# Kernel tuning notes

Measured on AMD Instinct MI355X. Metric: run time of the kernel, lower is better.

The kernel has to match this reference:

```python
import jax, jax.numpy as jnp
import numpy as np

DECAY = 0.99
COMMIT = 0.25
EPS = 1e-5


def setup_inputs() -> dict:
    key = jax.random.key(0)
    k1, k2, k3 = jax.random.split(key, 3)
    B, H, W, D, K = 32, 32, 32, 64, 1024
    return {
        "z": jax.random.normal(k1, (B, H, W, D), dtype=jnp.float32),
        "embeddings": jax.random.normal(k2, (K, D), dtype=jnp.float32),
        "cluster_size": jnp.ones((K,), dtype=jnp.float32),
        "ema_embed": jax.random.normal(k3, (K, D), dtype=jnp.float32),
    }


def reference(z, embeddings, cluster_size, ema_embed):
    B, H, W, D = z.shape
    K = embeddings.shape[0]
    z_flat = z.reshape(-1, D)                      # [N, D]

    # squared L2 distances via expansion: ||z||^2 + ||e||^2 - 2 z e^T  -> [N, K]
    distances = (
        jnp.sum(z_flat * z_flat, axis=1, keepdims=True)
        + jnp.sum(embeddings * embeddings, axis=1)
        - 2.0 * z_flat @ embeddings.T
    )
    idx = jnp.argmin(distances, axis=1)            # [N]
    quantized = embeddings[idx].reshape(z.shape)   # gather, [B,H,W,D]

    # training-mode EMA update (one_hot^T matmuls expressed as segment sums)
    n_i = jax.ops.segment_sum(jnp.ones(z_flat.shape[0], z.dtype), idx, num_segments=K)
    dw = jax.ops.segment_sum(z_flat, idx, num_segments=K)          # [K, D]
    new_cluster = cluster_size * DECAY + n_i * (1.0 - DECAY)
    new_ema = ema_embed * DECAY + dw * (1.0 - DECAY)
    n = jnp.sum(new_cluster)
    new_cluster = (new_cluster + EPS) / (n + K * EPS) * n           # Laplace smoothing
    new_embeddings = new_ema / new_cluster[:, None]

    loss = COMMIT * jnp.mean((z - jax.lax.stop_gradient(quantized)) ** 2)
    q_ste = z + jax.lax.stop_gradient(quantized - z)                # straight-through

    quantized_vectors = jnp.transpose(q_ste, (0, 3, 1, 2))          # [B, D, H, W]
    quantized_indices = idx.reshape(B, H, W)[:, None, :, :]         # [B, 1, H, W]
    return quantized_vectors, quantized_indices, loss, new_embeddings, new_cluster, new_ema
```

## Files before the change

### kernel.cpp

```cpp
#include <hip/hip_runtime.h>


typedef unsigned short u16;
typedef u16 us8 __attribute__((ext_vector_type(8)));
typedef float f4 __attribute__((ext_vector_type(4)));

#define WS_FZ    0
#define WS_FE    1
#define WS_FCS   2
#define WS_FEMA  3
#define WS_LOSS  4
#define WS_CSSUM 5

__device__ __forceinline__ float b2f(u16 u) {
    union { unsigned int i; float f; } x; x.i = ((unsigned int)u) << 16; return x.f;
}
__device__ __forceinline__ int swzE32(int d, int c) {
    return d * 32 + (c ^ ((((d) >> 2) & 7) << 2));
}
__device__ __forceinline__ int swzZ(int d, int c) {
    int cb = (c >> 2) ^ (c >> 5);
    int cc = ((cb & 31) << 2) | (c & 3);
    return d * 128 + (cc ^ ((((d) >> 2) & 7) << 2));
}

__global__ __launch_bounds__(256) void k_init(
    const u16* z, const u16* e, const u16* cs, const u16* ema,
    float* __restrict__ ws, float* __restrict__ esqp,
    float* __restrict__ dwp, long long zeroN, int K)
{
    __shared__ int flg[4];
    __shared__ float csred[256];
    const int tid = threadIdx.x;
    const int w = tid >> 6, l = tid & 63;
    const u16* p = (w == 0) ? z : (w == 1) ? e : (w == 2) ? cs : ema;
    int cnt = 0;
    #pragma unroll
    for (int t = 0; t < 4; ++t) {
        unsigned hb = (p[(l * 4 + t) * 2] >> 8) & 0x7F;
        cnt += (hb >= 0x3A && hb <= 0x41) ? 1 : 0;
    }
    #pragma unroll
    for (int off = 32; off; off >>= 1) cnt += __shfl_down(cnt, off);
    if (l == 0) flg[w] = (cnt < 128) ? 1 : 0;
    __syncthreads();
    if (blockIdx.x == 0) {
        if (tid < 4) ((int*)ws)[tid] = flg[tid];
        if (tid == 4) ws[WS_LOSS] = 0.0f;
    }
    const int fe = flg[1];
    const int fcs = flg[2];

    {
        const int gwave = (blockIdx.x * 256 + tid) >> 6;
        const int nwave = (gridDim.x * 256) >> 6;
        for (int code = gwave; code < K; code += nwave) {
            float v = fe ? ((const float*)e)[(size_t)code * 64 + l]
                         : b2f(e[(size_t)code * 64 + l]);
            float pq = v * v;
            asm volatile("" : "+v"(pq));
            float r[8];
            #pragma unroll
            for (int j = 0; j < 8; ++j) r[j] = __shfl(pq, j);
            #pragma unroll
            for (int t = 1; t < 8; ++t)
                #pragma unroll
                for (int j = 0; j < 8; ++j) r[j] += __shfl(pq, 8 * t + j);
            float s = ((r[0] + r[1]) + (r[2] + r[3])) + ((r[4] + r[5]) + (r[6] + r[7]));
            if (l == 0) esqp[code] = s;
        }
    }
    {
        long long g = (long long)blockIdx.x * 256 + tid;
        long long stride = (long long)gridDim.x * 256;
        for (long long i = g; i < zeroN; i += stride) dwp[i] = 0.0f;
    }
    if (blockIdx.x == 0) {
        float partial = 0.f;
        for (int k0 = tid; k0 < K; k0 += 256)
            partial += fcs ? ((const float*)cs)[k0] : b2f(cs[k0]);
        csred[tid] = partial;
        __syncthreads();
        for (int s = 128; s; s >>= 1) {
            if (tid < s) csred[tid] += csred[tid + s];
            __syncthreads();
        }
        if (tid == 0) ws[WS_CSSUM] = csred[0];
    }
}

__global__ __launch_bounds__(512, 4) void k_main(
    const u16* __restrict__ z, const u16* __restrict__ e,
    const float* __restrict__ esqp,
    float* __restrict__ ws, float* __restrict__ out,
    float* __restrict__ dwp,
    int K, int offIdx, long long outSize)
{
    __shared__ __align__(16) float z_t[64 * 128];
    __shared__ __align__(16) float e_t[4 * 32 * 64];
    __shared__ float esq_l[2048];
    __shared__ float z2_l[64];
    __shared__ int   idx_l[64];

    const int tid = threadIdx.x;
    const int cg  = tid >> 7;
    const int lt  = tid & 127;
    const int mtg = lt & 15;
    const int ktg = lt >> 4;
    const int pbase = blockIdx.x * 64;
    const int* wsi = (const int*)ws;
    const int fz = wsi[WS_FZ];
    const int fe = wsi[WS_FE];
    const int h = K >> 7;

    for (int i = tid; i < K; i += 512) esq_l[i] = esqp[i];

    if (fz) {
        const f4* z4 = (const f4*)((const float*)z + (size_t)pbase * 64);
        for (int i = tid; i < 1024; i += 512) {
            f4 v = z4[i];
            int m = i >> 4, d4 = (i & 15) * 4;
            z_t[swzZ(d4 + 0, m)] = v[0];
            z_t[swzZ(d4 + 1, m)] = v[1];
            z_t[swzZ(d4 + 2, m)] = v[2];
            z_t[swzZ(d4 + 3, m)] = v[3];
        }
    } else {
        const us8* z8 = (const us8*)(z + (size_t)pbase * 64);
        for (int i = tid; i < 512; i += 512) {
            us8 v = z8[i];
            int m = i >> 3, d8 = (i & 7) * 8;
            #pragma unroll
            for (int t = 0; t < 8; ++t) z_t[swzZ(d8 + t, m)] = b2f(v[t]);
        }
    }
    __syncthreads();
    if (tid < 64) {
        float r[8];
        #pragma unroll
        for (int j = 0; j < 8; ++j) {
            float v = z_t[swzZ(j, tid)]; float p = v * v;
            asm volatile("" : "+v"(p)); r[j] = p;
        }
        #pragma unroll
        for (int t = 1; t < 8; ++t)
            #pragma unroll
            for (int j = 0; j < 8; ++j) {
                float v = z_t[swzZ(8 * t + j, tid)]; float p = v * v;
                asm volatile("" : "+v"(p)); r[j] += p;
            }
        z2_l[tid] = ((r[0] + r[1]) + (r[2] + r[3])) + ((r[4] + r[5]) + (r[6] + r[7]));
    }

    float bestd[4] = {INFINITY, INFINITY, INFINITY, INFINITY};
    int   besti[4] = {0, 0, 0, 0};
    float* et = e_t + cg * 2048;

    f4  fb[4];
    us8 hb[2];
    {
        int kc0 = cg * h;
        if (fe) {
            const f4* e4 = (const f4*)((const float*)e + (size_t)kc0 * 2048);
            #pragma unroll
            for (int t = 0; t < 4; ++t) fb[t] = e4[lt + 128 * t];
        } else {
            const us8* e8 = (const us8*)(e + (size_t)kc0 * 2048);
            #pragma unroll
            for (int t = 0; t < 2; ++t) hb[t] = e8[lt + 128 * t];
        }
    }

    for (int c = 0; c < h; ++c) {
        const int kc = cg * h + c;
        if (fe) {
            #pragma unroll
            for (int t = 0; t < 4; ++t) {
                int i = lt + 128 * t;
                int kl = i >> 4, d4 = (i & 15) * 4;
                et[swzE32(d4 + 0, kl)] = fb[t][0];
                et[swzE32(d4 + 1, kl)] = fb[t][1];
                et[swzE32(d4 + 2, kl)] = fb[t][2];
                et[swzE32(d4 + 3, kl)] = fb[t][3];
            }
        } else {
            #pragma unroll
            for (int t = 0; t < 2; ++t) {
                int i = lt + 128 * t;
                int kl = i >> 3, d8 = (i & 7) * 8;
                #pragma unroll
                for (int s = 0; s < 8; ++s) et[swzE32(d8 + s, kl)] = b2f(hb[t][s]);
            }
        }
        if (c + 1 < h) {
            if (fe) {
                const f4* e4 = (const f4*)((const float*)e + (size_t)(kc + 1) * 2048);
                #pragma unroll
                for (int t = 0; t < 4; ++t) fb[t] = e4[lt + 128 * t];
            } else {
                const us8* e8 = (const us8*)(e + (size_t)(kc + 1) * 2048);
                #pragma unroll
                for (int t = 0; t < 2; ++t) hb[t] = e8[lt + 128 * t];
            }
        }
        __syncthreads();

        float acc[4][4] = {};
        for (int d0 = 0; d0 < 64; d0 += 4) {
            f4 za[4], ea[4];
            #pragma unroll
            for (int j = 0; j < 4; ++j) {
                int d = d0 + j;
                za[j] = *(const f4*)&z_t[swzZ(d, mtg * 4)];
                ea[j] = *(const f4*)&et[swzE32(d, ktg * 4)];
            }
            #pragma unroll
            for (int j = 0; j < 4; ++j) {
                #pragma unroll
                for (int a = 0; a < 4; ++a)
                    #pragma unroll
                    for (int b = 0; b < 4; ++b)
                        acc[a][b] += za[j][a] * ea[j][b];
            }
        }
        __syncthreads();

        #pragma unroll
        for (int a = 0; a < 4; ++a) {
            float z2 = z2_l[mtg * 4 + a];
            #pragma unroll
            for (int b = 0; b < 4; ++b) {
                float e2 = esq_l[kc * 32 + ktg * 4 + b];
                float dist = (z2 + e2) - 2.0f * acc[a][b];
                int kg = kc * 32 + ktg * 4 + b;
                if (dist < bestd[a]) { bestd[a] = dist; besti[a] = kg; }
            }
        }
    }

    __syncthreads();

    #pragma unroll
    for (int mask = 16; mask <= 32; mask <<= 1) {
        #pragma unroll
        for (int a = 0; a < 4; ++a) {
            float od = __shfl_xor(bestd[a], mask);
            int   oi = __shfl_xor(besti[a], mask);
            if (od < bestd[a] || (od == bestd[a] && oi < besti[a])) {
                bestd[a] = od; besti[a] = oi;
            }
        }
    }
    float* red_d = esq_l;
    int*   red_i = (int*)(esq_l + 576);
    if ((lt & 63) < 16) {
        int slot = cg * 2 + (lt >> 6);
        #pragma unroll
        for (int a = 0; a < 4; ++a) {
            red_d[(mtg * 4 + a) * 9 + slot] = bestd[a];
            red_i[(mtg * 4 + a) * 9 + slot] = besti[a];
        }
    }
    __syncthreads();

    if (tid < 64) {
        float bd = red_d[tid * 9]; int bi = red_i[tid * 9];
        #pragma unroll
        for (int t = 1; t < 8; ++t) {
            float dv = red_d[tid * 9 + t]; int iv = red_i[tid * 9 + t];
            if (dv < bd || (dv == bd && iv < bi)) { bd = dv; bi = iv; }
        }
        idx_l[tid] = bi;
        long long oi = (long long)offIdx + pbase + tid;
        if (oi < outSize) out[oi] = (float)bi;
    }
    __syncthreads();

    const int m = tid & 63;
    const int w = tid >> 6;
    const int p = pbase + m;
    const int b = p >> 10;
    const int hw = p & 1023;
    const int kidx = idx_l[m];
    float* zt2 = e_t;
    float lsum = 0.f;
    #pragma unroll
    for (int dd = 0; dd < 8; ++dd) {
        int d = w + 8 * dd;
        float zv = z_t[swzZ(d, m)];
        float q  = fe ? ((const float*)e)[(size_t)kidx * 64 + d]
                      : b2f(e[(size_t)kidx * 64 + d]);
        float df = zv - q;
        lsum += df * df;
        float qs = zv + (q - zv);
        long long qi = (long long)b * 65536 + d * 1024 + hw;
        if (qi < outSize) out[qi] = qs;
        zt2[m * 65 + d] = zv;
    }
    #pragma unroll
    for (int off = 32; off; off >>= 1) lsum += __shfl_down(lsum, off);
    if ((tid & 63) == 0) atomicAdd(&ws[WS_LOSS], lsum);
    __syncthreads();

    {
        const int wv = tid >> 6, lane = tid & 63;
        #pragma unroll
        for (int it = 0; it < 8; ++it) {
            int mm = wv * 8 + it;
            int kk = idx_l[mm];
            float zv = zt2[mm * 65 + lane];
            atomicAdd(&dwp[(size_t)kk * 64 + lane], zv);
            if (lane == 0) atomicAdd(&dwp[(size_t)K * 64 + kk], 1.0f);
        }
    }
}

__global__ __launch_bounds__(256) void k_fin(
    const u16* __restrict__ cs, const u16* __restrict__ ema,
    const float* __restrict__ ws, const float* __restrict__ dwp,
    float* __restrict__ out, int K, int N,
    long long offLoss, long long outSize, float lossScale)
{
    const int* wsi = (const int*)ws;
    const int fcs = wsi[WS_FCS], fema = wsi[WS_FEMA];
    const int i = blockIdx.x * 256 + threadIdx.x;
    const long long offEmb = offLoss + 1;
    const long long offCl  = offEmb + (long long)K * 64;
    const long long offEma = offCl + K;
    const float nsum = 0.99f * ws[WS_CSSUM] + 0.01f * (float)N;
    const float keps = (float)K * 1e-5f;

    float cnt = 0.f, dw = 0.f, csv = 0.f, ev = 0.f;
    int k = 0, d = 0;
    const int ok = (i < K * 64);
    if (ok) {
        k = i >> 6; d = i & 63;
        dw  = dwp[i];
        cnt = dwp[(size_t)K * 64 + k];
        csv = fcs ? ((const float*)cs)[k] : b2f(cs[k]);
        ev  = fema ? ((const float*)ema)[i] : b2f(ema[i]);
    }
    __syncthreads();
    if (ok) {
        float c  = csv * 0.99f + cnt * 0.01f;
        float sm = (c + 1e-5f) / (nsum + keps) * nsum;
        float ne = ev * 0.99f + dw * 0.01f;
        if (offEma + i < outSize) out[offEma + i] = ne;
        if (offEmb + i < outSize) out[offEmb + i] = ne / sm;
        if (d == 0 && offCl + k < outSize) out[offCl + k] = sm;
    }
    if (blockIdx.x == 0 && threadIdx.x == 0 && offLoss < outSize)
        out[offLoss] = 0.25f * (ws[WS_LOSS] * lossScale);
}

extern "C" void kernel_launch(void* const* d_in, const int* in_sizes, int n_in,
                              void* d_out, int out_size, void* d_ws, size_t ws_size,
                              hipStream_t stream) {
    long long sz[4] = {0, 0, 0, 0};
    for (int i = 0; i < n_in && i < 4; ++i) sz[i] = in_sizes[i];
    int icl = 0, iz = 0;
    for (int i = 1; i < 4; ++i) { if (sz[i] < sz[icl]) icl = i; if (sz[i] > sz[iz]) iz = i; }
    int ip[2], np = 0;
    for (int i = 0; i < 4; ++i) if (i != icl && i != iz && np < 2) ip[np++] = i;
    long long K = sz[icl], KD = (np == 2) ? sz[ip[0]] : 0;
    int derivOK = (n_in == 4 && np == 2 && icl != iz && sz[ip[0]] == sz[ip[1]] &&
                   K > 0 && KD % K == 0);
    long long D = derivOK ? KD / K : 64;
    long long N = (derivOK && D > 0 && sz[iz] % D == 0) ? sz[iz] / D : 32768;
    int ie, iema;
    if (!derivOK) { iz = 0; ie = 1; icl = 2; iema = 3; N = 32768; K = 1024; D = 64; }
    else if (icl > ip[0] && icl < ip[1]) { ie = ip[0]; iema = ip[1]; }
    else { iema = ip[0]; ie = ip[1]; }

    int fastOK = (D == 64) && (N % 1024 == 0) && (K % 256 == 0) &&
                 (K >= 512) && (K <= 2048);
    if (!fastOK) { N = 32768; K = 1024; }

    long long offIdx = N * 64, offLoss = offIdx + N;
    long long offEmb = offLoss + 1, offCl = offEmb + K * 64, offEma = offCl + K;

    float* out = (float*)d_out;
    float* ws = (float*)d_ws;

    long long rep = K * 65;
    float *esqp, *dwp;
    if ((long long)ws_size >= (8 + K + rep) * 4) {
        esqp = ws + 8; dwp = ws + 8 + K;
    } else {
        esqp = out + offEma; dwp = out + offEmb;
    }

    const u16* z   = (const u16*)d_in[iz];
    const u16* e   = (const u16*)d_in[ie];
    const u16* cs  = (const u16*)d_in[icl];
    const u16* ema = (const u16*)d_in[iema];

    float lossScale = (float)(1.0 / (double)(N * 64));

    k_init<<<64, 256, 0, stream>>>(z, e, cs, ema, ws, esqp, dwp, rep, (int)K);
    k_main<<<(int)(N / 64), 512, 0, stream>>>(z, e, esqp, ws, out, dwp,
                                              (int)K, (int)offIdx, (long long)out_size);
    k_fin<<<(int)((K * 64 + 255) / 256), 256, 0, stream>>>(cs, ema, ws, dwp, out,
                                                           (int)K, (int)N, offLoss,
                                                           (long long)out_size, lossScale);
}
```

Baseline: 170.9 us.

## Give each wavefront its own codebook slice to drop per-chunk block barriers

The codebook split moves from four 128-thread groups handling 32-entry chunks to eight 64-lane wavefronts, each owning a private 16-entry staging tile. Since each tile is written and read only by its own wavefront, the two __syncthreads per chunk iteration are removed, and single barriers are added after the z-norm computation and before the cross-wave reduction. Chunk count per wave doubles and each chunk has half the codebook columns, so per-chunk loads and argmin updates are amortised over less math. Correctness relies on lockstep execution within a wavefront in place of explicit barriers around the LDS tile.

```diff
diff --git a/kernel.cpp b/kernel.cpp
--- a/kernel.cpp
+++ b/kernel.cpp
@@ -15,8 +15,8 @@
 __device__ __forceinline__ float b2f(u16 u) {
     union { unsigned int i; float f; } x; x.i = ((unsigned int)u) << 16; return x.f;
 }
-__device__ __forceinline__ int swzE32(int d, int c) {
-    return d * 32 + (c ^ ((((d) >> 2) & 7) << 2));
+__device__ __forceinline__ int swz16(int d, int c) {
+    return d * 16 + (c ^ ((((d) >> 2) & 3) << 2));
 }
 __device__ __forceinline__ int swzZ(int d, int c) {
     int cb = (c >> 2) ^ (c >> 5);
@@ -97,16 +97,16 @@
     int K, int offIdx, long long outSize)
 {
     __shared__ __align__(16) float z_t[64 * 128];
-    __shared__ __align__(16) float e_t[4 * 32 * 64];
+    __shared__ __align__(16) float e_t[8 * 16 * 64];
     __shared__ float esq_l[2048];
     __shared__ float z2_l[64];
     __shared__ int   idx_l[64];
 
     const int tid = threadIdx.x;
-    const int cg  = tid >> 7;
-    const int lt  = tid & 127;
-    const int mtg = lt & 15;
-    const int ktg = lt >> 4;
+    const int wv  = tid >> 6;
+    const int lane = tid & 63;
+    const int mtg = lane & 15;
+    const int ktg = lane >> 4;
     const int pbase = blockIdx.x * 64;
     const int* wsi = (const int*)ws;
     const int fz = wsi[WS_FZ];
@@ -151,59 +151,57 @@
             }
         z2_l[tid] = ((r[0] + r[1]) + (r[2] + r[3])) + ((r[4] + r[5]) + (r[6] + r[7]));
     }
+    __syncthreads();
 
     float bestd[4] = {INFINITY, INFINITY, INFINITY, INFINITY};
     int   besti[4] = {0, 0, 0, 0};
-    float* et = e_t + cg * 2048;
+    float* et = e_t + wv * 1024;
+    const int kc0 = wv * h;
 
     f4  fb[4];
     us8 hb[2];
-    {
-        int kc0 = cg * h;
+    if (fe) {
+        const f4* e4 = (const f4*)((const float*)e + (size_t)kc0 * 1024);
+        #pragma unroll
+        for (int t = 0; t < 4; ++t) fb[t] = e4[lane + 64 * t];
+    } else {
+        const us8* e8 = (const us8*)(e + (size_t)kc0 * 1024);
+        #pragma unroll
+        for (int t = 0; t < 2; ++t) hb[t] = e8[lane + 64 * t];
+    }
+
+    for (int c = 0; c < h; ++c) {
+        const int kc = kc0 + c;
         if (fe) {
-            const f4* e4 = (const f4*)((const float*)e + (size_t)kc0 * 2048);
-            #pragma unroll
-            for (int t = 0; t < 4; ++t) fb[t] = e4[lt + 128 * t];
+            #pragma unroll
+            for (int t = 0; t < 4; ++t) {
+                int i = lane + 64 * t;
+                int kl = i >> 4, d4 = (i & 15) * 4;
+                et[swz16(d4 + 0, kl)] = fb[t][0];
+                et[swz16(d4 + 1, kl)] = fb[t][1];
+                et[swz16(d4 + 2, kl)] = fb[t][2];
+                et[swz16(d4 + 3, kl)] = fb[t][3];
+            }
         } else {
-            const us8* e8 = (const us8*)(e + (size_t)kc0 * 2048);
-            #pragma unroll
-            for (int t = 0; t < 2; ++t) hb[t] = e8[lt + 128 * t];
-        }
-    }
-
-    for (int c = 0; c < h; ++c) {
-        const int kc = cg * h + c;
-        if (fe) {
-            #pragma unroll
-            for (int t = 0; t < 4; ++t) {
-                int i = lt + 128 * t;
-                int kl = i >> 4, d4 = (i & 15) * 4;
-                et[swzE32(d4 + 0, kl)] = fb[t][0];
-                et[swzE32(d4 + 1, kl)] = fb[t][1];
-                et[swzE32(d4 + 2, kl)] = fb[t][2];
-                et[swzE32(d4 + 3, kl)] = fb[t][3];
-            }
-        } else {
             #pragma unroll
             for (int t = 0; t < 2; ++t) {
-                int i = lt + 128 * t;
+                int i = lane + 64 * t;
                 int kl = i >> 3, d8 = (i & 7) * 8;
                 #pragma unroll
-                for (int s = 0; s < 8; ++s) et[swzE32(d8 + s, kl)] = b2f(hb[t][s]);
+                for (int s = 0; s < 8; ++s) et[swz16(d8 + s, kl)] = b2f(hb[t][s]);
             }
         }
         if (c + 1 < h) {
             if (fe) {
-                const f4* e4 = (const f4*)((const float*)e + (size_t)(kc + 1) * 2048);
+                const f4* e4 = (const f4*)((const float*)e + (size_t)(kc + 1) * 1024);
                 #pragma unroll
-                for (int t = 0; t < 4; ++t) fb[t] = e4[lt + 128 * t];
+                for (int t = 0; t < 4; ++t) fb[t] = e4[lane + 64 * t];
             } else {
-                const us8* e8 = (const us8*)(e + (size_t)(kc + 1) * 2048);
+                const us8* e8 = (const us8*)(e + (size_t)(kc + 1) * 1024);
                 #pragma unroll
-                for (int t = 0; t < 2; ++t) hb[t] = e8[lt + 128 * t];
-            }
-        }
-        __syncthreads();
+                for (int t = 0; t < 2; ++t) hb[t] = e8[lane + 64 * t];
+            }
+        }
 
         float acc[4][4] = {};
         for (int d0 = 0; d0 < 64; d0 += 4) {
@@ -212,7 +210,7 @@
             for (int j = 0; j < 4; ++j) {
                 int d = d0 + j;
                 za[j] = *(const f4*)&z_t[swzZ(d, mtg * 4)];
-                ea[j] = *(const f4*)&et[swzE32(d, ktg * 4)];
+                ea[j] = *(const f4*)&et[swz16(d, ktg * 4)];
             }
             #pragma unroll
             for (int j = 0; j < 4; ++j) {
@@ -223,22 +221,19 @@
                         acc[a][b] += za[j][a] * ea[j][b];
             }
         }
-        __syncthreads();
 
         #pragma unroll
         for (int a = 0; a < 4; ++a) {
             float z2 = z2_l[mtg * 4 + a];
             #pragma unroll
             for (int b = 0; b < 4; ++b) {
-                float e2 = esq_l[kc * 32 + ktg * 4 + b];
+                float e2 = esq_l[kc * 16 + ktg * 4 + b];
                 float dist = (z2 + e2) - 2.0f * acc[a][b];
-                int kg = kc * 32 + ktg * 4 + b;
+                int kg = kc * 16 + ktg * 4 + b;
                 if (dist < bestd[a]) { bestd[a] = dist; besti[a] = kg; }
             }
         }
     }
-
-    __syncthreads();
 
     #pragma unroll
     for (int mask = 16; mask <= 32; mask <<= 1) {
@@ -251,14 +246,15 @@
             }
         }
     }
+    __syncthreads();
+
     float* red_d = esq_l;
     int*   red_i = (int*)(esq_l + 576);
-    if ((lt & 63) < 16) {
-        int slot = cg * 2 + (lt >> 6);
+    if (lane < 16) {
         #pragma unroll
         for (int a = 0; a < 4; ++a) {
-            red_d[(mtg * 4 + a) * 9 + slot] = bestd[a];
-            red_i[(mtg * 4 + a) * 9 + slot] = besti[a];
+            red_d[(mtg * 4 + a) * 9 + wv] = bestd[a];
+            red_i[(mtg * 4 + a) * 9 + wv] = besti[a];
         }
     }
     __syncthreads();
@@ -303,7 +299,6 @@
     __syncthreads();
 
     {
-        const int wv = tid >> 6, lane = tid & 63;
         #pragma unroll
         for (int it = 0; it < 8; ++it) {
             int mm = wv * 8 + it;
```

Result: slower. 343.1 us (+100.7%).
